# Performance work log

Hardware: AMD Instinct MI355X
Metric: run time of the kernel (lower is better)

The kernel has to match this reference:

```python
import jax, jax.numpy as jnp
import numpy as np

# Module constants (from init_kwargs)
WIN = 256      # window_size
STRIDE = 128   # stride (overlapping windows -> merge averages overlaps)
HEADS = 16


def setup_inputs() -> dict:
    key = jax.random.key(0)
    ks = jax.random.split(key, 5)
    B, S, D = 4, 4096, 1024
    scale = 0.02
    return {
        "hidden_states": jax.random.normal(ks[0], (B, S, D), jnp.float32),
        "Wq": jax.random.normal(ks[1], (D, D), jnp.float32) * scale,
        "Wk": jax.random.normal(ks[2], (D, D), jnp.float32) * scale,
        "Wv": jax.random.normal(ks[3], (D, D), jnp.float32) * scale,
        "Wo": jax.random.normal(ks[4], (D, D), jnp.float32) * scale,
    }


def reference(hidden_states, Wq, Wk, Wv, Wo):
    B, S, D = hidden_states.shape
    H = HEADS
    dh = D // H
    nw = (S - WIN) // STRIDE + 1  # number of sliding windows

    # gather overlapping windows: idx[w, j] = w*STRIDE + j
    idx = jnp.arange(nw)[:, None] * STRIDE + jnp.arange(WIN)[None, :]
    win = hidden_states[:, idx]

    # per-window multi-head attention (mask within a window is all-visible)
    def proj(x, Wm):
        return jnp.einsum('bnwd,de->bnwe', x, Wm).reshape(B, nw, WIN, H, dh)

    q = proj(win, Wq)
    k = proj(win, Wk)
    v = proj(win, Wv)

    scores = jnp.einsum('bnqhd,bnkhd->bnhqk', q, k) / jnp.sqrt(jnp.asarray(dh, q.dtype))
    attn = jax.nn.softmax(scores, axis=-1)
    ctx = jnp.einsum('bnhqk,bnkhd->bnqhd', attn, v)
    ctx = ctx.reshape(B, nw, WIN, D)
    win_out = jnp.einsum('bnwd,de->bnwe', ctx, Wo)

    # scatter-merge with overlap averaging
    flat_idx = idx.reshape(-1)
    out = jnp.zeros((B, S, D), hidden_states.dtype).at[:, flat_idx].add(
        win_out.reshape(B, nw * WIN, D))
    count = jnp.zeros((S,), hidden_states.dtype).at[flat_idx].add(1.0)
    out = out / (count[None, :, None] + 1e-8)
    return out
```

## Files before the change

### kernel.cpp

```cpp
#include <hip/hip_runtime.h>

#define SEQ 4096
#define DIM 1024
#define NWIN 31
#define NHEAD 16
#define NT 16

typedef __attribute__((ext_vector_type(8))) short bf16x8;
typedef __attribute__((ext_vector_type(4))) float f32x4;

#define MFMA(a, b, c) __builtin_amdgcn_mfma_f32_16x16x32_bf16((a), (b), (c), 0, 0, 0)

__device__ __forceinline__ unsigned short f2bf(float f) {
  union { float f; unsigned u; } v; v.f = f;
  unsigned r = v.u + 0x7FFFu + ((v.u >> 16) & 1u);
  return (unsigned short)(r >> 16);
}
__device__ __forceinline__ float bf2f(unsigned short h) {
  union { unsigned u; float f; } v; v.u = ((unsigned)h) << 16;
  return v.f;
}
__device__ __forceinline__ unsigned cvtpk(float lo, float hi) {
  unsigned r;
  asm("v_cvt_pk_bf16_f32 %0, %1, %2" : "=v"(r) : "v"(lo), "v"(hi));
  return r;
}

__device__ __forceinline__ void gll16(const void* g, void* l) {
  __builtin_amdgcn_global_load_lds((const __attribute__((address_space(1))) unsigned*)g,
                                   (__attribute__((address_space(3))) unsigned*)l,
                                   16, 0, 0);
}


__global__ __launch_bounds__(256) void cast_x_k(const float* __restrict__ x,
                                                unsigned short* __restrict__ o) {
  size_t i = ((size_t)blockIdx.x * 256 + threadIdx.x) * 8;
  float4 a = *(const float4*)(x + i);
  float4 b = *(const float4*)(x + i + 4);
  union { unsigned short u[8]; uint4 v; } pk;
  pk.u[0] = f2bf(a.x); pk.u[1] = f2bf(a.y); pk.u[2] = f2bf(a.z); pk.u[3] = f2bf(a.w);
  pk.u[4] = f2bf(b.x); pk.u[5] = f2bf(b.y); pk.u[6] = f2bf(b.z); pk.u[7] = f2bf(b.w);
  *(uint4*)(o + i) = pk.v;
}

__global__ __launch_bounds__(256) void sum_ctx_k(const unsigned short* __restrict__ a,
                                                 const unsigned short* __restrict__ b,
                                                 unsigned short* __restrict__ o) {
  size_t i = ((size_t)blockIdx.x * 256 + threadIdx.x) * 8;
  union { unsigned short u[8]; uint4 v; } pa, pb, po;
  pa.v = *(const uint4*)(a + i);
  pb.v = *(const uint4*)(b + i);
#pragma unroll
  for (int j = 0; j < 8; ++j) po.u[j] = f2bf(bf2f(pa.u[j]) + bf2f(pb.u[j]));
  *(uint4*)(o + i) = po.v;
}

__global__ __launch_bounds__(256) void zero_ctxb_k(unsigned short* __restrict__ ctxB) {
  int gtid = blockIdx.x * 256 + threadIdx.x;
  int idx = gtid * 8;
  int srow = idx >> 10;
  int b = srow >> 8;
  int r = srow & 255;
  int seqrow = b * SEQ + ((r < 128) ? r : (3840 + r));
  uint4 z = {0, 0, 0, 0};
  *(uint4*)(ctxB + (size_t)seqrow * DIM + (idx & 1023)) = z;
}


__global__ __launch_bounds__(256) void tcast_w_k(const float* __restrict__ W0, const float* __restrict__ W1,
                                                 const float* __restrict__ W2, const float* __restrict__ W3,
                                                 unsigned short* __restrict__ Wt3,
                                                 unsigned short* __restrict__ WoT) {
  __shared__ float tile[64][65];
  const int bid = blockIdx.x;
  const int mat = bid >> 8;
  const int t = bid & 255;
  const int tr = (t >> 4) * 64, tc = (t & 15) * 64;
  const float* W = (mat == 0) ? W0 : (mat == 1) ? W1 : (mat == 2) ? W2 : W3;
  unsigned short* out = (mat < 3) ? (Wt3 + (size_t)mat * 1024 * 1024) : WoT;
  const float fscale = (mat == 0) ? 0.18033688011112042f : 1.0f;
  const int tid = threadIdx.x;
  const int rr = tid >> 4, cc = (tid & 15) << 2;
#pragma unroll
  for (int i = 0; i < 4; ++i) {
    int r = i * 16 + rr;
    float4 v = *(const float4*)(W + (size_t)(tr + r) * DIM + tc + cc);
    tile[r][cc] = v.x; tile[r][cc + 1] = v.y; tile[r][cc + 2] = v.z; tile[r][cc + 3] = v.w;
  }
  __syncthreads();
#pragma unroll
  for (int i = 0; i < 4; ++i) {
    int orow = i * 16 + rr;
    union { unsigned short u[4]; uint2 v; } pk;
#pragma unroll
    for (int j = 0; j < 4; ++j) pk.u[j] = f2bf(tile[cc + j][orow] * fscale);
    *(uint2*)(out + (size_t)(tc + orow) * DIM + tr + cc) = pk.v;
  }
}


__device__ __forceinline__ void stage_half(const unsigned short* __restrict__ src,
                                           int row0, int kcol0, char* slot, int tid) {
  const int w = tid >> 6;
  const int r0 = tid >> 2;
  const int c = (((tid & 3) ^ ((tid >> 3) & 3))) * 8;
  gll16(src + (size_t)(row0 + r0) * DIM + kcol0 + c, slot + w * 1024);
  gll16(src + (size_t)(row0 + 128 + r0) * DIM + kcol0 + c, slot + 8192 + w * 1024);
}

__device__ __forceinline__ void gemm256_core(const unsigned short* __restrict__ A,
                                             const unsigned short* __restrict__ Bt,
                                             int m0, int n0, char* lds,
                                             f32x4 acc[8][4], int tid) {
  const int lane = tid & 63, w = tid >> 6;
  const int wm = w >> 2, wn = w & 3;
  const int l15 = lane & 15, g = lane >> 4;
  const int gs = g ^ ((l15 >> 1) & 3);

#define ASLOT(b, kk) (lds + ((b) * 2 + (kk)) * 16384)
#define BSLOT(b, kk) (lds + 65536 + ((b) * 2 + (kk)) * 16384)

  const int aoff = (wm * 128 + l15) * 64 + gs * 16;
  const int boff = (wn * 64 + l15) * 64 + gs * 16;

  stage_half(A,  m0, 0,  ASLOT(0, 0), tid);
  stage_half(Bt, n0, 0,  BSLOT(0, 0), tid);
  stage_half(A,  m0, 32, ASLOT(0, 1), tid);
  stage_half(Bt, n0, 32, BSLOT(0, 1), tid);
  stage_half(A,  m0, 64, ASLOT(1, 0), tid);
  stage_half(Bt, n0, 64, BSLOT(1, 0), tid);
  asm volatile("s_waitcnt vmcnt(8)" ::: "memory");
  __builtin_amdgcn_s_barrier();

  for (int s = 0; s < NT; ++s) {
    const int b = s & 1, nb = b ^ 1;
    const int k1 = (s + 1 < NT ? s + 1 : NT - 1) * 64;
    const int k2 = (s + 2 < NT ? s + 2 : NT - 1) * 64;
    char* Ab0 = ASLOT(b, 0); char* Ab1 = ASLOT(b, 1);
    char* Bb0 = BSLOT(b, 0); char* Bb1 = BSLOT(b, 1);
    bf16x8 af[8], bq0, bq1;

#pragma unroll
    for (int mt = 0; mt < 8; ++mt) af[mt] = *(const bf16x8*)(Ab0 + aoff + mt * 1024);
    bq0 = *(const bf16x8*)(Bb0 + boff);
    bq1 = *(const bf16x8*)(Bb0 + boff + 1024);
    stage_half(A, m0, k1 + 32, ASLOT(nb, 1), tid);
    __builtin_amdgcn_s_barrier();
    asm volatile("s_waitcnt lgkmcnt(0)" ::: "memory");
    __builtin_amdgcn_sched_barrier(0);
    __builtin_amdgcn_s_setprio(1);
#pragma unroll
    for (int mt = 0; mt < 8; ++mt) {
      acc[mt][0] = MFMA(af[mt], bq0, acc[mt][0]);
      acc[mt][1] = MFMA(af[mt], bq1, acc[mt][1]);
    }
    __builtin_amdgcn_s_setprio(0);

    bq0 = *(const bf16x8*)(Bb0 + boff + 2048);
    bq1 = *(const bf16x8*)(Bb0 + boff + 3072);
    stage_half(Bt, n0, k1 + 32, BSLOT(nb, 1), tid);
    asm volatile("s_waitcnt vmcnt(8)" ::: "memory");
    __builtin_amdgcn_s_barrier();
    asm volatile("s_waitcnt lgkmcnt(0)" ::: "memory");
    __builtin_amdgcn_sched_barrier(0);
    __builtin_amdgcn_s_setprio(1);
#pragma unroll
    for (int mt = 0; mt < 8; ++mt) {
      acc[mt][2] = MFMA(af[mt], bq0, acc[mt][2]);
      acc[mt][3] = MFMA(af[mt], bq1, acc[mt][3]);
    }
    __builtin_amdgcn_s_setprio(0);

#pragma unroll
    for (int mt = 0; mt < 8; ++mt) af[mt] = *(const bf16x8*)(Ab1 + aoff + mt * 1024);
    bq0 = *(const bf16x8*)(Bb1 + boff);
    bq1 = *(const bf16x8*)(Bb1 + boff + 1024);
    stage_half(A, m0, k2, ASLOT(b, 0), tid);
    __builtin_amdgcn_s_barrier();
    asm volatile("s_waitcnt lgkmcnt(0)" ::: "memory");
    __builtin_amdgcn_sched_barrier(0);
    __builtin_amdgcn_s_setprio(1);
#pragma unroll
    for (int mt = 0; mt < 8; ++mt) {
      acc[mt][0] = MFMA(af[mt], bq0, acc[mt][0]);
      acc[mt][1] = MFMA(af[mt], bq1, acc[mt][1]);
    }
    __builtin_amdgcn_s_setprio(0);

    bq0 = *(const bf16x8*)(Bb1 + boff + 2048);
    bq1 = *(const bf16x8*)(Bb1 + boff + 3072);
    stage_half(Bt, n0, k2, BSLOT(b, 0), tid);
    asm volatile("s_waitcnt vmcnt(8)" ::: "memory");
    __builtin_amdgcn_s_barrier();
    asm volatile("s_waitcnt lgkmcnt(0)" ::: "memory");
    __builtin_amdgcn_sched_barrier(0);
    __builtin_amdgcn_s_setprio(1);
#pragma unroll
    for (int mt = 0; mt < 8; ++mt) {
      acc[mt][2] = MFMA(af[mt], bq0, acc[mt][2]);
      acc[mt][3] = MFMA(af[mt], bq1, acc[mt][3]);
    }
    __builtin_amdgcn_s_setprio(0);
  }
#undef ASLOT
#undef BSLOT
}


__global__ __launch_bounds__(512, 2) void gemm_qkv_k(const unsigned short* __restrict__ Xb,
                                                     const unsigned short* __restrict__ Wt3,
                                                     unsigned short* __restrict__ Qb,
                                                     unsigned short* __restrict__ Kb,
                                                     unsigned short* __restrict__ Vt) {
  __shared__ char lds[131072];
  const int nwg = 768;
  const int wg = blockIdx.x;
  const int swz = (wg & 7) * (nwg >> 3) + (wg >> 3);
  const int mtile = swz / 12, ntile = swz % 12;
  const int m0 = mtile * 256, n0 = ntile * 256;
  const int tid = threadIdx.x;

  f32x4 acc[8][4] = {};
  gemm256_core(Xb, Wt3, m0, n0, lds, acc, tid);

  const int lane = tid & 63, w = tid >> 6;
  const int wm = w >> 2, wn = w & 3;
  const int l15 = lane & 15, g = lane >> 4;
  const int mg0 = m0 + wm * 128;
  const int ng0 = n0 + wn * 64;

  if (n0 < 2048) {
    unsigned short* O = (n0 < 1024) ? Qb : Kb;
    const int nb = (n0 < 1024) ? 0 : 1024;
#pragma unroll
    for (int mt = 0; mt < 8; ++mt)
#pragma unroll
      for (int nt = 0; nt < 4; ++nt) {
        int ng = ng0 + nt * 16 + l15 - nb;
        int mg = mg0 + mt * 16 + g * 4;
#pragma unroll
        for (int r = 0; r < 4; ++r)
          O[(size_t)(mg + r) * DIM + ng] = f2bf(acc[mt][nt][r]);
      }
  } else {
#pragma unroll
    for (int mt = 0; mt < 8; ++mt)
#pragma unroll
      for (int nt = 0; nt < 4; ++nt) {
        int ng = ng0 + nt * 16 + l15 - 2048;
        int mg = mg0 + mt * 16 + g * 4;
        union { unsigned short u[4]; uint2 v; } pk;
#pragma unroll
        for (int r = 0; r < 4; ++r) pk.u[r] = f2bf(acc[mt][nt][r]);
        *(uint2*)(Vt + (size_t)ng * (4 * SEQ) + mg) = pk.v;
      }
  }
}


__global__ __launch_bounds__(512, 2) void gemm_out_k(const unsigned short* __restrict__ Cs,
                                                     const unsigned short* __restrict__ WoT,
                                                     float* __restrict__ out) {
  __shared__ char lds[131072];
  const int nwg = 256;
  const int wg = blockIdx.x;
  const int swz = (wg & 7) * (nwg >> 3) + (wg >> 3);
  const int mtile = swz >> 2, ntile = swz & 3;
  const int m0 = mtile * 256, n0 = ntile * 256;
  const int tid = threadIdx.x;

  f32x4 acc[8][4] = {};
  gemm256_core(Cs, WoT, m0, n0, lds, acc, tid);

  const int lane = tid & 63, w = tid >> 6;
  const int wm = w >> 2, wn = w & 3;
  const int l15 = lane & 15, g = lane >> 4;
  const int mg0 = m0 + wm * 128;
  const int ng0 = n0 + wn * 64;
#pragma unroll
  for (int mt = 0; mt < 8; ++mt)
#pragma unroll
    for (int nt = 0; nt < 4; ++nt) {
      int ng = ng0 + nt * 16 + l15;
      int mg = mg0 + mt * 16 + g * 4;
#pragma unroll
      for (int r = 0; r < 4; ++r) {
        int m = mg + r;
        int s = m & (SEQ - 1);
        float scl = (s < 128 || s >= SEQ - 128) ? 1.0f : 0.5f;
        out[(size_t)m * DIM + ng] = acc[mt][nt][r] * scl;
      }
    }
}


__global__ __launch_bounds__(512, 4) void attn_k(const unsigned short* __restrict__ Qb,
                                                 const unsigned short* __restrict__ Kb,
                                                 const unsigned short* __restrict__ Vt,
                                                 unsigned short* __restrict__ ctxA,
                                                 unsigned short* __restrict__ ctxB) {
  __shared__ char Kls[32768];
  __shared__ char Vls[32768];

  const int bid = blockIdx.x;
  const int h = bid & 15;
  const int rem = bid >> 4;
  const int n = rem % NWIN;
  const int b = rem / NWIN;
  const int tid = threadIdx.x;
  const int lane = tid & 63;
  const int w = tid >> 6;
  const int l15 = lane & 15, g = lane >> 4;

  const size_t qkbase = ((size_t)b * SEQ + (size_t)n * 128) * DIM + h * 64;
  const int wdst = w * 1024;

  {
    const int kr0 = tid >> 3;
    const int ksc = ((tid & 7) ^ (kr0 & 7)) * 8;
    const unsigned short* kg = Kb + qkbase + (size_t)kr0 * DIM + ksc;
#pragma unroll
    for (int j = 0; j < 4; ++j)
      gll16(kg + (size_t)(64 * j) * DIM, Kls + 8192 * j + wdst);
  }
  {
    const int vr0 = tid >> 5;
    const int vsc = ((tid & 31) ^ (vr0 & 7)) * 8;
    const unsigned short* vg = Vt + (size_t)(h * 64 + vr0) * (4 * SEQ) +
                               (size_t)b * SEQ + n * 128 + vsc;
#pragma unroll
    for (int j = 0; j < 4; ++j)
      gll16(vg + (size_t)(16 * j) * (4 * SEQ), Vls + 8192 * j + wdst);
  }

  bf16x8 qf[2][2];
#pragma unroll
  for (int qt = 0; qt < 2; ++qt)
#pragma unroll
    for (int kf = 0; kf < 2; ++kf)
      qf[qt][kf] = *(const bf16x8*)(Qb + qkbase +
                                    (size_t)(w * 32 + qt * 16 + l15) * DIM + kf * 32 + g * 8);

  __syncthreads();

  f32x4 acc[2][4] = {};
  f32x4 psv[2] = {};

  for (int kc = 0; kc < 4; ++kc) {
    f32x4 s0[4] = {}, s1[4] = {};
#pragma unroll
    for (int kt = 0; kt < 4; ++kt) {
      int row = kc * 64 + kt * 16 + l15;
      bf16x8 k0 = *(const bf16x8*)(Kls + row * 128 + ((g ^ (row & 7)) << 4));
      bf16x8 k1 = *(const bf16x8*)(Kls + row * 128 + (((4 + g) ^ (row & 7)) << 4));
      s0[kt] = MFMA(k0, qf[0][0], s0[kt]);
      s0[kt] = MFMA(k1, qf[0][1], s0[kt]);
      s1[kt] = MFMA(k0, qf[1][0], s1[kt]);
      s1[kt] = MFMA(k1, qf[1][1], s1[kt]);
    }
#pragma unroll
    for (int kt = 0; kt < 4; ++kt) {
#pragma unroll
      for (int r = 0; r < 4; ++r) {
        s0[kt][r] = exp2f(s0[kt][r]);
        s1[kt][r] = exp2f(s1[kt][r]);
      }
      psv[0] += s0[kt];
      psv[1] += s1[kt];
    }
    union { unsigned u[4]; bf16x8 v; } pa[2][2];
#pragma unroll
    for (int c = 0; c < 2; ++c) {
      pa[0][c].u[0] = cvtpk(s0[2 * c][0], s0[2 * c][1]);
      pa[0][c].u[1] = cvtpk(s0[2 * c][2], s0[2 * c][3]);
      pa[0][c].u[2] = cvtpk(s0[2 * c + 1][0], s0[2 * c + 1][1]);
      pa[0][c].u[3] = cvtpk(s0[2 * c + 1][2], s0[2 * c + 1][3]);
      pa[1][c].u[0] = cvtpk(s1[2 * c][0], s1[2 * c][1]);
      pa[1][c].u[1] = cvtpk(s1[2 * c][2], s1[2 * c][3]);
      pa[1][c].u[2] = cvtpk(s1[2 * c + 1][0], s1[2 * c + 1][1]);
      pa[1][c].u[3] = cvtpk(s1[2 * c + 1][2], s1[2 * c + 1][3]);
    }
#pragma unroll
    for (int c = 0; c < 2; ++c)
#pragma unroll
      for (int dt = 0; dt < 4; ++dt) {
        int row = dt * 16 + l15;
        int c16 = kc * 8 + c * 4 + (g >> 1);
        int off = (g & 1) * 8;
        union { uint2 u2[2]; bf16x8 v; } vv;
        vv.u2[0] = *(const uint2*)(Vls + row * 512 + ((c16 ^ (row & 7)) << 4) + off);
        vv.u2[1] = *(const uint2*)(Vls + row * 512 + (((c16 + 2) ^ (row & 7)) << 4) + off);
        acc[0][dt] = MFMA(vv.v, pa[0][c].v, acc[0][dt]);
        acc[1][dt] = MFMA(vv.v, pa[1][c].v, acc[1][dt]);
      }
  }

  unsigned short* outb = (n & 1) ? ctxB : ctxA;
  const size_t obase = ((size_t)b * SEQ + (size_t)n * 128 + w * 32) * DIM + h * 64;
#pragma unroll
  for (int qt = 0; qt < 2; ++qt) {
    float ps = psv[qt][0] + psv[qt][1] + psv[qt][2] + psv[qt][3];
    ps += __shfl_xor(ps, 16);
    ps += __shfl_xor(ps, 32);
    float inv = 1.0f / ps;
#pragma unroll
    for (int dt = 0; dt < 4; ++dt) {
      union { unsigned short u[4]; uint2 v; } pk;
#pragma unroll
      for (int r = 0; r < 4; ++r) pk.u[r] = f2bf(acc[qt][dt][r] * inv);
      *(uint2*)(outb + obase + (size_t)(qt * 16 + l15) * DIM + dt * 16 + g * 4) = pk.v;
    }
  }
}


extern "C" void kernel_launch(void* const* d_in, const int* in_sizes, int n_in,
                              void* d_out, int out_size, void* d_ws, size_t ws_size,
                              hipStream_t stream) {
  const float* X  = (const float*)d_in[0];
  const float* Wq = (const float*)d_in[1];
  const float* Wk = (const float*)d_in[2];
  const float* Wv = (const float*)d_in[3];
  const float* Wo = (const float*)d_in[4];
  float* out = (float*)d_out;

  char* ws = (char*)d_ws;
  const size_t SZ = (size_t)4 * SEQ * DIM * 2;
  unsigned short* Xb   = (unsigned short*)(ws);
  unsigned short* Wt3  = (unsigned short*)(ws + SZ);
  unsigned short* WoT  = (unsigned short*)(ws + SZ + 6291456);
  unsigned short* Qb   = (unsigned short*)(ws + SZ + 8388608);
  unsigned short* Kb   = (unsigned short*)(ws + 2 * SZ + 8388608);
  unsigned short* Vt   = (unsigned short*)(ws + 3 * SZ + 8388608);
  unsigned short* ctxA = (unsigned short*)(ws + 4 * SZ + 8388608);
  unsigned short* ctxB = (unsigned short*)(ws + 5 * SZ + 8388608);

  zero_ctxb_k<<<512, 256, 0, stream>>>(ctxB);
  cast_x_k<<<8192, 256, 0, stream>>>(X, Xb);
  tcast_w_k<<<1024, 256, 0, stream>>>(Wq, Wk, Wv, Wo, Wt3, WoT);
  gemm_qkv_k<<<768, 512, 0, stream>>>(Xb, Wt3, Qb, Kb, Vt);
  attn_k<<<4 * NWIN * NHEAD, 512, 0, stream>>>(Qb, Kb, Vt, ctxA, ctxB);
  sum_ctx_k<<<8192, 256, 0, stream>>>(ctxA, ctxB, Xb );
  gemm_out_k<<<256, 512, 0, stream>>>(Xb, WoT, out);
}
```

Before: 257.2 us.

## Fuse ctxA+ctxB sum into output GEMM A-tile loading; add setprio in attention

Removes the separate sum_ctx_k pass by having the output projection GEMM load both context buffers through registers, add them in bf16 pairs, and write the summed tile into LDS. This drops one full read/write round trip of a 32 MB intermediate and a kernel launch. In exchange, the A operand now goes through VGPRs instead of direct global-to-LDS loads, so each tile costs twice the A global reads plus extra ALU and register pressure. It also adds s_setprio around the MFMA blocks in the attention kernel.

Result: no change. 254.7 us (-1.0%).

```diff
diff --git a/kernel.cpp b/kernel.cpp
--- a/kernel.cpp
+++ b/kernel.cpp
@@ -24,6 +24,12 @@
   unsigned r;
   asm("v_cvt_pk_bf16_f32 %0, %1, %2" : "=v"(r) : "v"(lo), "v"(hi));
   return r;
+}
+__device__ __forceinline__ unsigned addbf2(unsigned x, unsigned y) {
+  union { unsigned u; float f; } a, b, c, d;
+  a.u = x << 16; b.u = x & 0xffff0000u;
+  c.u = y << 16; d.u = y & 0xffff0000u;
+  return cvtpk(a.f + c.f, b.f + d.f);
 }
 
 __device__ __forceinline__ void gll16(const void* g, void* l) {
@@ -42,18 +48,6 @@
   pk.u[0] = f2bf(a.x); pk.u[1] = f2bf(a.y); pk.u[2] = f2bf(a.z); pk.u[3] = f2bf(a.w);
   pk.u[4] = f2bf(b.x); pk.u[5] = f2bf(b.y); pk.u[6] = f2bf(b.z); pk.u[7] = f2bf(b.w);
   *(uint4*)(o + i) = pk.v;
-}
-
-__global__ __launch_bounds__(256) void sum_ctx_k(const unsigned short* __restrict__ a,
-                                                 const unsigned short* __restrict__ b,
-                                                 unsigned short* __restrict__ o) {
-  size_t i = ((size_t)blockIdx.x * 256 + threadIdx.x) * 8;
-  union { unsigned short u[8]; uint4 v; } pa, pb, po;
-  pa.v = *(const uint4*)(a + i);
-  pb.v = *(const uint4*)(b + i);
-#pragma unroll
-  for (int j = 0; j < 8; ++j) po.u[j] = f2bf(bf2f(pa.u[j]) + bf2f(pb.u[j]));
-  *(uint4*)(o + i) = po.v;
 }
 
 __global__ __launch_bounds__(256) void zero_ctxb_k(unsigned short* __restrict__ ctxB) {
@@ -208,6 +202,137 @@
 }
 
 
+struct AR { uint4 a0, b0, a1, b1; };
+
+__device__ __forceinline__ void issueA(const unsigned short* __restrict__ cA,
+                                       const unsigned short* __restrict__ cB,
+                                       int row0, int kcol0, int tid, AR& r) {
+  const int r0 = tid >> 2;
+  const int c = (((tid & 3) ^ ((tid >> 3) & 3))) * 8;
+  const size_t o1 = (size_t)(row0 + r0) * DIM + kcol0 + c;
+  const size_t o2 = (size_t)(row0 + 128 + r0) * DIM + kcol0 + c;
+  r.a0 = *(const uint4*)(cA + o1);
+  r.b0 = *(const uint4*)(cB + o1);
+  r.a1 = *(const uint4*)(cA + o2);
+  r.b1 = *(const uint4*)(cB + o2);
+}
+
+__device__ __forceinline__ void writeA(char* slot, int tid, const AR& r) {
+  uint4 lo, hi;
+  lo.x = addbf2(r.a0.x, r.b0.x); lo.y = addbf2(r.a0.y, r.b0.y);
+  lo.z = addbf2(r.a0.z, r.b0.z); lo.w = addbf2(r.a0.w, r.b0.w);
+  hi.x = addbf2(r.a1.x, r.b1.x); hi.y = addbf2(r.a1.y, r.b1.y);
+  hi.z = addbf2(r.a1.z, r.b1.z); hi.w = addbf2(r.a1.w, r.b1.w);
+  *(uint4*)(slot + tid * 16) = lo;
+  *(uint4*)(slot + 8192 + tid * 16) = hi;
+}
+
+__device__ __forceinline__ void gemm256_core_sum(const unsigned short* __restrict__ cA,
+                                                 const unsigned short* __restrict__ cB,
+                                                 const unsigned short* __restrict__ Bt,
+                                                 int m0, int n0, char* lds,
+                                                 f32x4 acc[8][4], int tid) {
+  const int lane = tid & 63, w = tid >> 6;
+  const int wm = w >> 2, wn = w & 3;
+  const int l15 = lane & 15, g = lane >> 4;
+  const int gs = g ^ ((l15 >> 1) & 3);
+
+#define ASLOT(b, kk) (lds + ((b) * 2 + (kk)) * 16384)
+#define BSLOT(b, kk) (lds + 65536 + ((b) * 2 + (kk)) * 16384)
+
+  const int aoff = (wm * 128 + l15) * 64 + gs * 16;
+  const int boff = (wn * 64 + l15) * 64 + gs * 16;
+
+  AR R0, R1;
+  issueA(cA, cB, m0, 0, tid, R0);  writeA(ASLOT(0, 0), tid, R0);
+  issueA(cA, cB, m0, 32, tid, R0); writeA(ASLOT(0, 1), tid, R0);
+  issueA(cA, cB, m0, 64, tid, R0); writeA(ASLOT(1, 0), tid, R0);
+  stage_half(Bt, n0, 0,  BSLOT(0, 0), tid);
+  stage_half(Bt, n0, 32, BSLOT(0, 1), tid);
+  stage_half(Bt, n0, 64, BSLOT(1, 0), tid);
+  issueA(cA, cB, m0, 96, tid, R1);
+  asm volatile("s_waitcnt vmcnt(8)" ::: "memory");
+  asm volatile("s_waitcnt lgkmcnt(0)" ::: "memory");
+  __builtin_amdgcn_s_barrier();
+
+  for (int s = 0; s < NT; ++s) {
+    const int b = s & 1, nb = b ^ 1;
+    const int k1 = (s + 1 < NT ? s + 1 : NT - 1) * 64;
+    const int k2 = (s + 2 < NT ? s + 2 : NT - 1) * 64;
+    char* Ab0 = ASLOT(b, 0); char* Ab1 = ASLOT(b, 1);
+    char* Bb0 = BSLOT(b, 0); char* Bb1 = BSLOT(b, 1);
+    bf16x8 af[8], bq0, bq1;
+    (void)k1;
+
+    writeA(ASLOT(nb, 1), tid, R1);
+    issueA(cA, cB, m0, k2, tid, R0);
+#pragma unroll
+    for (int mt = 0; mt < 8; ++mt) af[mt] = *(const bf16x8*)(Ab0 + aoff + mt * 1024);
+    bq0 = *(const bf16x8*)(Bb0 + boff);
+    bq1 = *(const bf16x8*)(Bb0 + boff + 1024);
+    __builtin_amdgcn_s_barrier();
+    asm volatile("s_waitcnt lgkmcnt(0)" ::: "memory");
+    __builtin_amdgcn_sched_barrier(0);
+    __builtin_amdgcn_s_setprio(1);
+#pragma unroll
+    for (int mt = 0; mt < 8; ++mt) {
+      acc[mt][0] = MFMA(af[mt], bq0, acc[mt][0]);
+      acc[mt][1] = MFMA(af[mt], bq1, acc[mt][1]);
+    }
+    __builtin_amdgcn_s_setprio(0);
+
+    bq0 = *(const bf16x8*)(Bb0 + boff + 2048);
+    bq1 = *(const bf16x8*)(Bb0 + boff + 3072);
+    stage_half(Bt, n0, k1 + 32, BSLOT(nb, 1), tid);
+    asm volatile("s_waitcnt vmcnt(8)" ::: "memory");
+    __builtin_amdgcn_s_barrier();
+    asm volatile("s_waitcnt lgkmcnt(0)" ::: "memory");
+    __builtin_amdgcn_sched_barrier(0);
+    __builtin_amdgcn_s_setprio(1);
+#pragma unroll
+    for (int mt = 0; mt < 8; ++mt) {
+      acc[mt][2] = MFMA(af[mt], bq0, acc[mt][2]);
+      acc[mt][3] = MFMA(af[mt], bq1, acc[mt][3]);
+    }
+    __builtin_amdgcn_s_setprio(0);
+
+    writeA(ASLOT(b, 0), tid, R0);
+    issueA(cA, cB, m0, k2 + 32, tid, R1);
+#pragma unroll
+    for (int mt = 0; mt < 8; ++mt) af[mt] = *(const bf16x8*)(Ab1 + aoff + mt * 1024);
+    bq0 = *(const bf16x8*)(Bb1 + boff);
+    bq1 = *(const bf16x8*)(Bb1 + boff + 1024);
+    __builtin_amdgcn_s_barrier();
+    asm volatile("s_waitcnt lgkmcnt(0)" ::: "memory");
+    __builtin_amdgcn_sched_barrier(0);
+    __builtin_amdgcn_s_setprio(1);
+#pragma unroll
+    for (int mt = 0; mt < 8; ++mt) {
+      acc[mt][0] = MFMA(af[mt], bq0, acc[mt][0]);
+      acc[mt][1] = MFMA(af[mt], bq1, acc[mt][1]);
+    }
+    __builtin_amdgcn_s_setprio(0);
+
+    bq0 = *(const bf16x8*)(Bb1 + boff + 2048);
+    bq1 = *(const bf16x8*)(Bb1 + boff + 3072);
+    stage_half(Bt, n0, k2, BSLOT(b, 0), tid);
+    asm volatile("s_waitcnt vmcnt(8)" ::: "memory");
+    __builtin_amdgcn_s_barrier();
+    asm volatile("s_waitcnt lgkmcnt(0)" ::: "memory");
+    __builtin_amdgcn_sched_barrier(0);
+    __builtin_amdgcn_s_setprio(1);
+#pragma unroll
+    for (int mt = 0; mt < 8; ++mt) {
+      acc[mt][2] = MFMA(af[mt], bq0, acc[mt][2]);
+      acc[mt][3] = MFMA(af[mt], bq1, acc[mt][3]);
+    }
+    __builtin_amdgcn_s_setprio(0);
+  }
+#undef ASLOT
+#undef BSLOT
+}
+
+
 __global__ __launch_bounds__(512, 2) void gemm_qkv_k(const unsigned short* __restrict__ Xb,
                                                      const unsigned short* __restrict__ Wt3,
                                                      unsigned short* __restrict__ Qb,
@@ -259,7 +384,8 @@
 }
 
 
-__global__ __launch_bounds__(512, 2) void gemm_out_k(const unsigned short* __restrict__ Cs,
+__global__ __launch_bounds__(512, 2) void gemm_out_k(const unsigned short* __restrict__ cA,
+                                                     const unsigned short* __restrict__ cB,
                                                      const unsigned short* __restrict__ WoT,
                                                      float* __restrict__ out) {
   __shared__ char lds[131072];
@@ -271,7 +397,7 @@
   const int tid = threadIdx.x;
 
   f32x4 acc[8][4] = {};
-  gemm256_core(Cs, WoT, m0, n0, lds, acc, tid);
+  gemm256_core_sum(cA, cB, WoT, m0, n0, lds, acc, tid);
 
   const int lane = tid & 63, w = tid >> 6;
   const int wm = w >> 2, wn = w & 3;
@@ -349,6 +475,7 @@
 
   for (int kc = 0; kc < 4; ++kc) {
     f32x4 s0[4] = {}, s1[4] = {};
+    __builtin_amdgcn_s_setprio(1);
 #pragma unroll
     for (int kt = 0; kt < 4; ++kt) {
       int row = kc * 64 + kt * 16 + l15;
@@ -359,6 +486,7 @@
       s1[kt] = MFMA(k0, qf[1][0], s1[kt]);
       s1[kt] = MFMA(k1, qf[1][1], s1[kt]);
     }
+    __builtin_amdgcn_s_setprio(0);
 #pragma unroll
     for (int kt = 0; kt < 4; ++kt) {
 #pragma unroll
@@ -381,6 +509,7 @@
       pa[1][c].u[2] = cvtpk(s1[2 * c + 1][0], s1[2 * c + 1][1]);
       pa[1][c].u[3] = cvtpk(s1[2 * c + 1][2], s1[2 * c + 1][3]);
     }
+    __builtin_amdgcn_s_setprio(1);
 #pragma unroll
     for (int c = 0; c < 2; ++c)
 #pragma unroll
@@ -394,6 +523,7 @@
         acc[0][dt] = MFMA(vv.v, pa[0][c].v, acc[0][dt]);
         acc[1][dt] = MFMA(vv.v, pa[1][c].v, acc[1][dt]);
       }
+    __builtin_amdgcn_s_setprio(0);
   }
 
   unsigned short* outb = (n & 1) ? ctxB : ctxA;
@@ -441,6 +571,5 @@
   tcast_w_k<<<1024, 256, 0, stream>>>(Wq, Wk, Wv, Wo, Wt3, WoT);
   gemm_qkv_k<<<768, 512, 0, stream>>>(Xb, Wt3, Qb, Kb, Vt);
   attn_k<<<4 * NWIN * NHEAD, 512, 0, stream>>>(Qb, Kb, Vt, ctxA, ctxB);
-  sum_ctx_k<<<8192, 256, 0, stream>>>(ctxA, ctxB, Xb );
-  gemm_out_k<<<256, 512, 0, stream>>>(Xb, WoT, out);
-}
+  gemm_out_k<<<256, 512, 0, stream>>>(ctxA, ctxB, WoT, out);
+}
```
